# Performance work log

Measured on AMD Instinct MI355X. Metric: run time of the kernel, lower is better.

Reference implementation:

```python
import jax, jax.numpy as jnp
import numpy as np

N = 50000
E = 800000
D_IN, D_H1, D_H2, D_OUT = 128, 128, 64, 32


def setup_inputs() -> dict:
    key = jax.random.key(0)
    ks = jax.random.split(key, 8)
    x = jax.random.normal(ks[0], (N, D_IN), dtype=jnp.float32)
    edge_index = jax.random.randint(ks[1], (2, E), 0, N, dtype=jnp.int64)
    # Glorot-ish init for GCNConv weights, zero bias (PyG default bias init is zeros)
    def glorot(k, fi, fo):
        lim = np.sqrt(6.0 / (fi + fo)).astype(np.float32)
        return jax.random.uniform(k, (fi, fo), dtype=jnp.float32, minval=-lim, maxval=lim)
    return {
        "x": x,
        "edge_index": edge_index,
        "W1": glorot(ks[2], D_IN, D_H1), "b1": jnp.zeros((D_H1,), jnp.float32),
        "W2": glorot(ks[3], D_H1, D_H2), "b2": jnp.zeros((D_H2,), jnp.float32),
        "W3": glorot(ks[4], D_H2, D_OUT), "b3": jnp.zeros((D_OUT,), jnp.float32),
    }


def _gcn_norm(edge_index, n):
    # add self-loops, then symmetric normalization D^{-1/2} (A+I) D^{-1/2}
    loop = jnp.arange(n, dtype=edge_index.dtype)
    src = jnp.concatenate([edge_index[0], loop])  # [E+N]
    dst = jnp.concatenate([edge_index[1], loop])
    deg = jax.ops.segment_sum(jnp.ones_like(dst, dtype=jnp.float32), dst, num_segments=n)
    dinv = jnp.where(deg > 0, jax.lax.rsqrt(jnp.maximum(deg, 1.0)), 0.0)
    norm = dinv[src] * dinv[dst]  # [E+N]
    return src, dst, norm


def _gcn_layer(x, W, b, src, dst, norm, n):
    h = x @ W                                   # [N, d_out]
    msg = h[src] * norm[:, None]                # gather + scale, [E+N, d_out]
    agg = jax.ops.segment_sum(msg, dst, num_segments=n)
    return agg + b


def reference(x, edge_index, W1, b1, W2, b2, W3, b3):
    n = x.shape[0]
    src, dst, norm = _gcn_norm(edge_index, n)   # cached=True: computed once
    h = jax.nn.relu(_gcn_layer(x, W1, b1, src, dst, norm, n))
    h = jax.nn.relu(_gcn_layer(h, W2, b2, src, dst, norm, n))
    return _gcn_layer(h, W3, b3, src, dst, norm, n)
```

## Files before the change

### kernel.cpp

```cpp
#include <hip/hip_runtime.h>
#include <hip/hip_bf16.h>
#include <cstdint>

using short8 = __attribute__((ext_vector_type(8))) short;
using f32x4  = __attribute__((ext_vector_type(4))) float;

constexpr int CAP = 8192;

__device__ __forceinline__ unsigned f2bf_bits(float f) {
    unsigned u = __float_as_uint(f);
    return (u + 0x7fffu + ((u >> 16) & 1u)) >> 16;
}
__device__ __forceinline__ float bf_lo(unsigned u) { return __uint_as_float(u << 16); }
__device__ __forceinline__ float bf_hi(unsigned u) { return __uint_as_float(u & 0xffff0000u); }


__device__ __forceinline__ void prepack_one(const float* __restrict__ W,
                                            short* __restrict__ Wh, short* __restrict__ Wl,
                                            int DOUT, int idx) {
    int lane = idx & 63, tile = idx >> 6;
    int NT = DOUT / 16;
    int kk = tile / NT, ct = tile - kk * NT;
    int g = lane >> 4, cl = lane & 15;
    int c = ct * 16 + cl;
    short8 h8, l8;
#pragma unroll
    for (int j = 0; j < 8; ++j) {
        float w = W[(size_t)(kk * 32 + g * 8 + j) * DOUT + c];
        unsigned hb = f2bf_bits(w);
        unsigned lb = f2bf_bits(w - bf_lo(hb));
        h8[j] = (short)hb; l8[j] = (short)lb;
    }
    *reinterpret_cast<short8*>(&Wh[(size_t)idx * 8]) = h8;
    *reinterpret_cast<short8*>(&Wl[(size_t)idx * 8]) = l8;
}

__global__ __launch_bounds__(256) void prepack_all_kernel(const float* __restrict__ W1,
                                                          const float* __restrict__ W2,
                                                          const float* __restrict__ W3,
                                                          short* __restrict__ w1h, short* __restrict__ w1l,
                                                          short* __restrict__ w2h, short* __restrict__ w2l,
                                                          short* __restrict__ w3h, short* __restrict__ w3l,
                                                          int* __restrict__ bkt_cursor) {
    int idx = blockIdx.x * 256 + threadIdx.x;
    if (idx < 2048)      prepack_one(W1, w1h, w1l, 128, idx);
    else if (idx < 3072) prepack_one(W2, w2h, w2l, 64,  idx - 2048);
    else if (idx < 3328) prepack_one(W3, w3h, w3l, 32,  idx - 3072);
    else if (idx < 3584) bkt_cursor[idx - 3328] = 0;
}


struct BinSh {
    int qcnt[256];
    int qofs[256];
    int gbase[256];
    uint2 staging[4096];
};
struct GemmSh {
    unsigned Xh[64 * 64];
    unsigned Xl[64 * 64];
};
union SharedU { BinSh b; GemmSh g; };

__global__ __launch_bounds__(512) void bin_gemm1_kernel(const int* __restrict__ src,
                                                        const int* __restrict__ dst, int E,
                                                        int* __restrict__ bkt_cursor,
                                                        unsigned* __restrict__ bin,
                                                        const float* __restrict__ X,
                                                        const short8* __restrict__ Wp_hi,
                                                        const short8* __restrict__ Wp_lo,
                                                        unsigned* __restrict__ G,
                                                        int n, int NBE) {
    __shared__ SharedU sh;
    const int t = threadIdx.x;

    if ((int)blockIdx.x < NBE) {
        const int e0 = (int)blockIdx.x * 4096;
        if (t < 256) sh.b.qcnt[t] = 0;
        __syncthreads();
        int sa[8], da[8], slot[8];
#pragma unroll
        for (int k = 0; k < 8; ++k) {
            int e = e0 + k * 512 + t;
            sa[k] = -1; da[k] = 0; slot[k] = 0;
            if (e < E) {
                int ss = src[e], dd = dst[e];
                if (ss >= 0 && ss < n && dd >= 0 && dd < n) {
                    sa[k] = ss; da[k] = dd;
                    slot[k] = atomicAdd(&sh.b.qcnt[dd >> 8], 1);
                }
            }
        }
        __syncthreads();
        if (t < 256) sh.b.qofs[t] = sh.b.qcnt[t];
        __syncthreads();
        for (int off = 1; off < 256; off <<= 1) {
            int val = 0;
            if (t < 256 && t >= off) val = sh.b.qofs[t - off];
            __syncthreads();
            if (t < 256) sh.b.qofs[t] += val;
            __syncthreads();
        }
        if (t < 256) {
            int myc = sh.b.qcnt[t];
            if (myc > 0) sh.b.gbase[t] = atomicAdd(&bkt_cursor[t], myc);
            sh.b.qofs[t] -= myc;
        }
        __syncthreads();
#pragma unroll
        for (int k = 0; k < 8; ++k) {
            if (sa[k] >= 0)
                sh.b.staging[sh.b.qofs[da[k] >> 8] + slot[k]] =
                    make_uint2((unsigned)sa[k], (unsigned)da[k]);
        }
        __syncthreads();
        const int tot = sh.b.qofs[255] + sh.b.qcnt[255];
        for (int i = t; i < tot; i += 512) {
            uint2 en = sh.b.staging[i];
            int b = (int)(en.y >> 8);
            int pos = sh.b.gbase[b] + (i - sh.b.qofs[b]);
            if (pos < CAP)
                bin[(size_t)b * CAP + pos] = ((en.y & 255u) << 24) | en.x;
        }
        return;
    }

    constexpr int NT = 8, NTW = 4, NK = 4, WPR = 64;
    const int row0 = ((int)blockIdx.x - NBE) * 64;

    for (int i = t * 4; i < 64 * 128; i += 2048) {
        int r = i / 128, c = i % 128;
        float4 v = make_float4(0.f, 0.f, 0.f, 0.f);
        if (row0 + r < n) v = *reinterpret_cast<const float4*>(&X[(size_t)(row0 + r) * 128 + c]);
        unsigned h0 = f2bf_bits(v.x), h1 = f2bf_bits(v.y), h2 = f2bf_bits(v.z), h3 = f2bf_bits(v.w);
        unsigned l0 = f2bf_bits(v.x - bf_lo(h0)), l1 = f2bf_bits(v.y - bf_lo(h1));
        unsigned l2 = f2bf_bits(v.z - bf_lo(h2)), l3 = f2bf_bits(v.w - bf_lo(h3));
        int w = (r * WPR + c / 2) ^ ((r & 7) << 2);
        *reinterpret_cast<uint2*>(&sh.g.Xh[w]) = make_uint2(h0 | (h1 << 16), h2 | (h3 << 16));
        *reinterpret_cast<uint2*>(&sh.g.Xl[w]) = make_uint2(l0 | (l1 << 16), l2 | (l3 << 16));
    }
    __syncthreads();

    const int lane = t & 63, wid = t >> 6;
    const int strip = wid >> 1, half = wid & 1;
    const int g = lane >> 4, cl = lane & 15;
    const int lrow = strip * 16 + cl;
    f32x4 acc[NTW];
#pragma unroll
    for (int i = 0; i < NTW; ++i) acc[i] = (f32x4){0.f, 0.f, 0.f, 0.f};

#pragma unroll
    for (int kk = 0; kk < NK; ++kk) {
        int wb = (lrow * WPR + kk * 16 + g * 4) ^ ((lrow & 7) << 2);
        short8 xh = *reinterpret_cast<const short8*>(&sh.g.Xh[wb]);
        short8 xl = *reinterpret_cast<const short8*>(&sh.g.Xl[wb]);
#pragma unroll
        for (int i = 0; i < NTW; ++i) {
            int ct = half * NTW + i;
            short8 wh = Wp_hi[(kk * NT + ct) * 64 + lane];
            short8 wl = Wp_lo[(kk * NT + ct) * 64 + lane];
            acc[i] = __builtin_amdgcn_mfma_f32_16x16x32_bf16(wh, xh, acc[i], 0, 0, 0);
            acc[i] = __builtin_amdgcn_mfma_f32_16x16x32_bf16(wh, xl, acc[i], 0, 0, 0);
            acc[i] = __builtin_amdgcn_mfma_f32_16x16x32_bf16(wl, xh, acc[i], 0, 0, 0);
        }
    }

    const int r = row0 + lrow;
    if (r < n) {
#pragma unroll
        for (int i = 0; i < NTW; ++i) {
            int c0 = (half * NTW + i) * 16 + g * 4;
            unsigned p0 = f2bf_bits(acc[i][0]) | (f2bf_bits(acc[i][1]) << 16);
            unsigned p1 = f2bf_bits(acc[i][2]) | (f2bf_bits(acc[i][3]) << 16);
            *reinterpret_cast<uint2*>(&G[(size_t)r * 64 + c0 / 2]) = make_uint2(p0, p1);
        }
    }
}

__global__ __launch_bounds__(256) void bucket_offsets_fill_kernel(const unsigned* __restrict__ bin,
                                                                  const int* __restrict__ bkt_cursor,
                                                                  int2* __restrict__ off2,
                                                                  float* __restrict__ dinv,
                                                                  int* __restrict__ csr, int n) {
    __shared__ int cnt[256];
    __shared__ int sh[256];
    __shared__ int cur[256];
    const int t = threadIdx.x;
    const int b = blockIdx.x;
    const int S = b * CAP;
    const int count = min(bkt_cursor[b], CAP);
    cnt[t] = 0;
    __syncthreads();
    for (int i = t; i < count; i += 256) atomicAdd(&cnt[bin[S + i] >> 24], 1);
    __syncthreads();
    const int c = cnt[t];
    sh[t] = c;
    __syncthreads();
    for (int off = 1; off < 256; off <<= 1) {
        int val = (t >= off) ? sh[t - off] : 0;
        __syncthreads();
        sh[t] += val;
        __syncthreads();
    }
    const int start = S + sh[t] - c;
    cur[t] = start;
    const int node = b * 256 + t;
    if (node < n) {
        off2[node] = make_int2(start, start + c);
        dinv[node] = rsqrtf((float)(c + 1));
    }
    __syncthreads();
    for (int i = t; i < count; i += 256) {
        unsigned p = bin[S + i];
        int pos = atomicAdd(&cur[p >> 24], 1);
        csr[pos] = (int)(p & 0xFFFFFFu);
    }
}


template<int DIN, int DOUT, bool SCALE_IN>
__global__ __launch_bounds__(512) void fused_agg_gemm_kernel(const unsigned* __restrict__ Gin,
                                                             const int2* __restrict__ off2,
                                                             const int* __restrict__ csr,
                                                             const float* __restrict__ dinv,
                                                             const float* __restrict__ bias,
                                                             const short8* __restrict__ Wp_hi,
                                                             const short8* __restrict__ Wp_lo,
                                                             unsigned* __restrict__ Gout, int n) {
    constexpr int NT    = DOUT / 16;
    constexpr int NTW   = NT / 2;
    constexpr int NK    = DIN / 32;
    constexpr int WPR   = DIN / 2;
    constexpr int W4    = DIN / 8;
    constexpr int LPN   = W4;
    constexpr int SLOTS = 512 / LPN;
    constexpr int ROUNDS = 64 / SLOTS;
    __shared__ unsigned Xh[64 * WPR];
    __shared__ unsigned Xl[64 * WPR];
    const int t = threadIdx.x;
    const int node0 = blockIdx.x * 64;
    const int slot = t / LPN, cw = t % LPN;
    const uint4* gB = reinterpret_cast<const uint4*>(Gin) + cw;
    const int col = cw * 8;
    const float4 bs0 = *reinterpret_cast<const float4*>(&bias[col]);
    const float4 bs1 = *reinterpret_cast<const float4*>(&bias[col + 4]);

#pragma unroll
    for (int rd = 0; rd < ROUNDS; ++rd) {
        const int r = rd * SLOTS + slot;
        const int v = node0 + r;
        unsigned hw[4] = {0u, 0u, 0u, 0u}, lw[4] = {0u, 0u, 0u, 0u};
        if (v < n) {
            const float dv = dinv[v];
            float a[8], b[8];
            uint4 us = gB[(size_t)v * W4];
            const float sself = SCALE_IN ? dv : 1.f;
            a[0] = sself * bf_lo(us.x); a[1] = sself * bf_hi(us.x);
            a[2] = sself * bf_lo(us.y); a[3] = sself * bf_hi(us.y);
            a[4] = sself * bf_lo(us.z); a[5] = sself * bf_hi(us.z);
            a[6] = sself * bf_lo(us.w); a[7] = sself * bf_hi(us.w);
#pragma unroll
            for (int q = 0; q < 8; ++q) b[q] = 0.f;
            const int2 se = off2[v];
            int j = se.x;
            for (; j + 4 <= se.y; j += 4) {
                int u0 = csr[j], u1 = csr[j + 1], u2 = csr[j + 2], u3 = csr[j + 3];
                uint4 x0 = gB[(size_t)u0 * W4];
                uint4 x1 = gB[(size_t)u1 * W4];
                uint4 x2 = gB[(size_t)u2 * W4];
                uint4 x3 = gB[(size_t)u3 * W4];
                if (SCALE_IN) {
                    float w0 = dinv[u0], w1 = dinv[u1], w2 = dinv[u2], w3 = dinv[u3];
                    a[0] = fmaf(w0, bf_lo(x0.x), a[0]); a[1] = fmaf(w0, bf_hi(x0.x), a[1]);
                    a[2] = fmaf(w0, bf_lo(x0.y), a[2]); a[3] = fmaf(w0, bf_hi(x0.y), a[3]);
                    a[4] = fmaf(w0, bf_lo(x0.z), a[4]); a[5] = fmaf(w0, bf_hi(x0.z), a[5]);
                    a[6] = fmaf(w0, bf_lo(x0.w), a[6]); a[7] = fmaf(w0, bf_hi(x0.w), a[7]);
                    b[0] = fmaf(w1, bf_lo(x1.x), b[0]); b[1] = fmaf(w1, bf_hi(x1.x), b[1]);
                    b[2] = fmaf(w1, bf_lo(x1.y), b[2]); b[3] = fmaf(w1, bf_hi(x1.y), b[3]);
                    b[4] = fmaf(w1, bf_lo(x1.z), b[4]); b[5] = fmaf(w1, bf_hi(x1.z), b[5]);
                    b[6] = fmaf(w1, bf_lo(x1.w), b[6]); b[7] = fmaf(w1, bf_hi(x1.w), b[7]);
                    a[0] = fmaf(w2, bf_lo(x2.x), a[0]); a[1] = fmaf(w2, bf_hi(x2.x), a[1]);
                    a[2] = fmaf(w2, bf_lo(x2.y), a[2]); a[3] = fmaf(w2, bf_hi(x2.y), a[3]);
                    a[4] = fmaf(w2, bf_lo(x2.z), a[4]); a[5] = fmaf(w2, bf_hi(x2.z), a[5]);
                    a[6] = fmaf(w2, bf_lo(x2.w), a[6]); a[7] = fmaf(w2, bf_hi(x2.w), a[7]);
                    b[0] = fmaf(w3, bf_lo(x3.x), b[0]); b[1] = fmaf(w3, bf_hi(x3.x), b[1]);
                    b[2] = fmaf(w3, bf_lo(x3.y), b[2]); b[3] = fmaf(w3, bf_hi(x3.y), b[3]);
                    b[4] = fmaf(w3, bf_lo(x3.z), b[4]); b[5] = fmaf(w3, bf_hi(x3.z), b[5]);
                    b[6] = fmaf(w3, bf_lo(x3.w), b[6]); b[7] = fmaf(w3, bf_hi(x3.w), b[7]);
                } else {
                    a[0] += bf_lo(x0.x); a[1] += bf_hi(x0.x); a[2] += bf_lo(x0.y); a[3] += bf_hi(x0.y);
                    a[4] += bf_lo(x0.z); a[5] += bf_hi(x0.z); a[6] += bf_lo(x0.w); a[7] += bf_hi(x0.w);
                    b[0] += bf_lo(x1.x); b[1] += bf_hi(x1.x); b[2] += bf_lo(x1.y); b[3] += bf_hi(x1.y);
                    b[4] += bf_lo(x1.z); b[5] += bf_hi(x1.z); b[6] += bf_lo(x1.w); b[7] += bf_hi(x1.w);
                    a[0] += bf_lo(x2.x); a[1] += bf_hi(x2.x); a[2] += bf_lo(x2.y); a[3] += bf_hi(x2.y);
                    a[4] += bf_lo(x2.z); a[5] += bf_hi(x2.z); a[6] += bf_lo(x2.w); a[7] += bf_hi(x2.w);
                    b[0] += bf_lo(x3.x); b[1] += bf_hi(x3.x); b[2] += bf_lo(x3.y); b[3] += bf_hi(x3.y);
                    b[4] += bf_lo(x3.z); b[5] += bf_hi(x3.z); b[6] += bf_lo(x3.w); b[7] += bf_hi(x3.w);
                }
            }
            for (; j < se.y; ++j) {
                int u0 = csr[j];
                uint4 x0 = gB[(size_t)u0 * W4];
                if (SCALE_IN) {
                    float w0 = dinv[u0];
                    a[0] = fmaf(w0, bf_lo(x0.x), a[0]); a[1] = fmaf(w0, bf_hi(x0.x), a[1]);
                    a[2] = fmaf(w0, bf_lo(x0.y), a[2]); a[3] = fmaf(w0, bf_hi(x0.y), a[3]);
                    a[4] = fmaf(w0, bf_lo(x0.z), a[4]); a[5] = fmaf(w0, bf_hi(x0.z), a[5]);
                    a[6] = fmaf(w0, bf_lo(x0.w), a[6]); a[7] = fmaf(w0, bf_hi(x0.w), a[7]);
                } else {
                    a[0] += bf_lo(x0.x); a[1] += bf_hi(x0.x); a[2] += bf_lo(x0.y); a[3] += bf_hi(x0.y);
                    a[4] += bf_lo(x0.z); a[5] += bf_hi(x0.z); a[6] += bf_lo(x0.w); a[7] += bf_hi(x0.w);
                }
            }
            const float bb[8] = {bs0.x, bs0.y, bs0.z, bs0.w, bs1.x, bs1.y, bs1.z, bs1.w};
#pragma unroll
            for (int q = 0; q < 8; ++q) {
                float o = fmaxf(dv * (a[q] + b[q]) + bb[q], 0.f);
                unsigned hb = f2bf_bits(o);
                unsigned lb = f2bf_bits(o - bf_lo(hb));
                hw[q >> 1] |= (q & 1) ? (hb << 16) : hb;
                lw[q >> 1] |= (q & 1) ? (lb << 16) : lb;
            }
        }
        const int w0 = (r * WPR + cw * 4) ^ ((r & 7) << 2);
        *reinterpret_cast<uint4*>(&Xh[w0]) = make_uint4(hw[0], hw[1], hw[2], hw[3]);
        *reinterpret_cast<uint4*>(&Xl[w0]) = make_uint4(lw[0], lw[1], lw[2], lw[3]);
    }
    __syncthreads();

    const int lane = t & 63, wid = t >> 6;
    const int strip = wid >> 1, half = wid & 1;
    const int g = lane >> 4, cl = lane & 15;
    const int lrow = strip * 16 + cl;
    f32x4 acc[NTW];
#pragma unroll
    for (int i = 0; i < NTW; ++i) acc[i] = (f32x4){0.f, 0.f, 0.f, 0.f};

#pragma unroll
    for (int kk = 0; kk < NK; ++kk) {
        int wb = (lrow * WPR + kk * 16 + g * 4) ^ ((lrow & 7) << 2);
        short8 xh = *reinterpret_cast<const short8*>(&Xh[wb]);
        short8 xl = *reinterpret_cast<const short8*>(&Xl[wb]);
#pragma unroll
        for (int i = 0; i < NTW; ++i) {
            int ct = half * NTW + i;
            short8 wh = Wp_hi[(kk * NT + ct) * 64 + lane];
            short8 wl = Wp_lo[(kk * NT + ct) * 64 + lane];
            acc[i] = __builtin_amdgcn_mfma_f32_16x16x32_bf16(wh, xh, acc[i], 0, 0, 0);
            acc[i] = __builtin_amdgcn_mfma_f32_16x16x32_bf16(wh, xl, acc[i], 0, 0, 0);
            acc[i] = __builtin_amdgcn_mfma_f32_16x16x32_bf16(wl, xh, acc[i], 0, 0, 0);
        }
    }

    const int r = node0 + lrow;
    if (r < n) {
        const float s = dinv[r];
#pragma unroll
        for (int i = 0; i < NTW; ++i) {
            int c0 = (half * NTW + i) * 16 + g * 4;
            unsigned p0 = f2bf_bits(acc[i][0] * s) | (f2bf_bits(acc[i][1] * s) << 16);
            unsigned p1 = f2bf_bits(acc[i][2] * s) | (f2bf_bits(acc[i][3] * s) << 16);
            *reinterpret_cast<uint2*>(&Gout[(size_t)r * (DOUT / 2) + c0 / 2]) = make_uint2(p0, p1);
        }
    }
}


__global__ __launch_bounds__(256) void aggregate_final_kernel(const unsigned* __restrict__ G,
                                                              const int2* __restrict__ off2,
                                                              const int* __restrict__ csr,
                                                              const float* __restrict__ dinv,
                                                              const float* __restrict__ bias,
                                                              float* __restrict__ out, int n) {
    constexpr int D = 32, W2u = 8, LPN = 8;
    const int t = threadIdx.x;
    const int v = blockIdx.x * 32 + t / LPN;
    if (v >= n) return;
    const int cw = t % LPN;
    const uint2* gB = reinterpret_cast<const uint2*>(G) + cw;

    float a[4], b[4];
    uint2 us = gB[(size_t)v * W2u];
    a[0] = bf_lo(us.x); a[1] = bf_hi(us.x); a[2] = bf_lo(us.y); a[3] = bf_hi(us.y);
#pragma unroll
    for (int q = 0; q < 4; ++q) b[q] = 0.f;

    const int2 se = off2[v];
    int j = se.x;
    for (; j + 4 <= se.y; j += 4) {
        uint2 x0 = gB[(size_t)csr[j]     * W2u];
        uint2 x1 = gB[(size_t)csr[j + 1] * W2u];
        uint2 x2 = gB[(size_t)csr[j + 2] * W2u];
        uint2 x3 = gB[(size_t)csr[j + 3] * W2u];
        a[0] += bf_lo(x0.x); a[1] += bf_hi(x0.x); a[2] += bf_lo(x0.y); a[3] += bf_hi(x0.y);
        b[0] += bf_lo(x1.x); b[1] += bf_hi(x1.x); b[2] += bf_lo(x1.y); b[3] += bf_hi(x1.y);
        a[0] += bf_lo(x2.x); a[1] += bf_hi(x2.x); a[2] += bf_lo(x2.y); a[3] += bf_hi(x2.y);
        b[0] += bf_lo(x3.x); b[1] += bf_hi(x3.x); b[2] += bf_lo(x3.y); b[3] += bf_hi(x3.y);
    }
    for (; j < se.y; ++j) {
        uint2 x0 = gB[(size_t)csr[j] * W2u];
        a[0] += bf_lo(x0.x); a[1] += bf_hi(x0.x); a[2] += bf_lo(x0.y); a[3] += bf_hi(x0.y);
    }

    const float dv = dinv[v];
    const int col = cw * 4;
    const float4 bs = *reinterpret_cast<const float4*>(&bias[col]);
    float4 o = make_float4(dv * (a[0] + b[0]) + bs.x, dv * (a[1] + b[1]) + bs.y,
                           dv * (a[2] + b[2]) + bs.z, dv * (a[3] + b[3]) + bs.w);
    *reinterpret_cast<float4*>(&out[(size_t)v * D + col]) = o;
}


extern "C" void kernel_launch(void* const* d_in, const int* in_sizes, int n_in,
                              void* d_out, int out_size, void* d_ws, size_t ws_size,
                              hipStream_t stream) {
    const int N = 50000, E = 800000;
    const int NB  = (N + 255) / 256;
    const int NBE = (E + 4095) / 4096;
    const int NG  = (N + 63) / 64;
    const float* x  = (const float*)d_in[0];
    const int* ei = (const int*)d_in[1];
    const int* src = ei;
    const int* dst = ei + E;
    const float* W1 = (const float*)d_in[2]; const float* b1 = (const float*)d_in[3];
    const float* W2 = (const float*)d_in[4]; const float* b2 = (const float*)d_in[5];
    const float* W3 = (const float*)d_in[6]; const float* b3 = (const float*)d_in[7];
    float* out = (float*)d_out;

    char* ws = (char*)d_ws;
    size_t off = 0;
    auto alloc = [&](size_t bytes) -> void* {
        void* p = ws + off;
        off = (off + bytes + 255) & ~(size_t)255;
        return p;
    };
    int2*     off2       = (int2*)alloc((size_t)N * 8);
    float*    dinv       = (float*)alloc((size_t)N * 4);
    int*      csr        = (int*)alloc((size_t)NB * CAP * 4);
    unsigned* bin        = (unsigned*)alloc((size_t)NB * CAP * 4);
    unsigned* g1         = (unsigned*)alloc((size_t)N * 64 * 4);
    unsigned* g2         = (unsigned*)alloc((size_t)N * 32 * 4);
    unsigned* g3         = (unsigned*)alloc((size_t)N * 16 * 4);
    int*      bkt_cursor = (int*)alloc((size_t)256 * 4);
    short*    wp1h = (short*)alloc((size_t)128 * 128 * 2);
    short*    wp1l = (short*)alloc((size_t)128 * 128 * 2);
    short*    wp2h = (short*)alloc((size_t)128 * 64 * 2);
    short*    wp2l = (short*)alloc((size_t)128 * 64 * 2);
    short*    wp3h = (short*)alloc((size_t)64 * 32 * 2);
    short*    wp3l = (short*)alloc((size_t)64 * 32 * 2);
    (void)ws_size; (void)n_in; (void)in_sizes; (void)out_size;

    prepack_all_kernel<<<14, 256, 0, stream>>>(W1, W2, W3, wp1h, wp1l, wp2h, wp2l, wp3h, wp3l,
                                               bkt_cursor);
    bin_gemm1_kernel<<<NBE + NG, 512, 0, stream>>>(src, dst, E, bkt_cursor, bin,
                                                   x, (const short8*)wp1h, (const short8*)wp1l,
                                                   g1, N, NBE);
    bucket_offsets_fill_kernel<<<NB, 256, 0, stream>>>(bin, bkt_cursor, off2, dinv, csr, N);
    fused_agg_gemm_kernel<128, 64, true><<<NG, 512, 0, stream>>>(g1, off2, csr, dinv, b1,
                                                                 (const short8*)wp2h,
                                                                 (const short8*)wp2l, g2, N);
    fused_agg_gemm_kernel<64, 32, false><<<NG, 512, 0, stream>>>(g2, off2, csr, dinv, b2,
                                                                 (const short8*)wp3h,
                                                                 (const short8*)wp3l, g3, N);
    aggregate_final_kernel<<<(N * 8 + 255) / 256, 256, 0, stream>>>(g3, off2, csr, dinv, b3, out, N);
}
```

Measured before the change: 115.6 us.

## Prescale layer-1 features by dinv in bucket kernel; unroll gathers by eight

The bucket/offset kernel now multiplies each g1 row by its source-node dinv and writes it back as bf16, right after computing degrees. This removes the per-edge dinv gather and FMA scaling from the first fused aggregation, so both fused layers share one unscaled add path. The gather loops in the fused and final aggregation kernels are unrolled from 4 to 8 neighbours to keep more loads in flight. The cost is an extra read-modify-write pass over g1, a second bf16 rounding of the prescaled values, and higher register pressure from the wider unroll.

```diff
diff --git a/kernel.cpp b/kernel.cpp
--- a/kernel.cpp
+++ b/kernel.cpp
@@ -181,10 +181,12 @@
                                                                   const int* __restrict__ bkt_cursor,
                                                                   int2* __restrict__ off2,
                                                                   float* __restrict__ dinv,
-                                                                  int* __restrict__ csr, int n) {
+                                                                  int* __restrict__ csr,
+                                                                  unsigned* __restrict__ g1, int n) {
     __shared__ int cnt[256];
     __shared__ int sh[256];
     __shared__ int cur[256];
+    __shared__ float sdinv[256];
     const int t = threadIdx.x;
     const int b = blockIdx.x;
     const int S = b * CAP;
@@ -204,10 +206,13 @@
     }
     const int start = S + sh[t] - c;
     cur[t] = start;
-    const int node = b * 256 + t;
+    const float dv = rsqrtf((float)(c + 1));
+    sdinv[t] = dv;
+    const int node0 = b * 256;
+    const int node = node0 + t;
     if (node < n) {
         off2[node] = make_int2(start, start + c);
-        dinv[node] = rsqrtf((float)(c + 1));
+        dinv[node] = dv;
     }
     __syncthreads();
     for (int i = t; i < count; i += 256) {
@@ -215,10 +220,21 @@
         int pos = atomicAdd(&cur[p >> 24], 1);
         csr[pos] = (int)(p & 0xFFFFFFu);
     }
-}
-
-
-template<int DIN, int DOUT, bool SCALE_IN>
+    const int rows = min(256, n - node0);
+    uint4* g4 = reinterpret_cast<uint4*>(g1 + (size_t)node0 * 64);
+    for (int i = t; i < rows * 16; i += 256) {
+        const float s = sdinv[i >> 4];
+        uint4 v = g4[i];
+        unsigned r0 = f2bf_bits(s * bf_lo(v.x)) | (f2bf_bits(s * bf_hi(v.x)) << 16);
+        unsigned r1 = f2bf_bits(s * bf_lo(v.y)) | (f2bf_bits(s * bf_hi(v.y)) << 16);
+        unsigned r2 = f2bf_bits(s * bf_lo(v.z)) | (f2bf_bits(s * bf_hi(v.z)) << 16);
+        unsigned r3 = f2bf_bits(s * bf_lo(v.w)) | (f2bf_bits(s * bf_hi(v.w)) << 16);
+        g4[i] = make_uint4(r0, r1, r2, r3);
+    }
+}
+
+
+template<int DIN, int DOUT>
 __global__ __launch_bounds__(512) void fused_agg_gemm_kernel(const unsigned* __restrict__ Gin,
                                                              const int2* __restrict__ off2,
                                                              const int* __restrict__ csr,
@@ -251,67 +267,54 @@
         const int v = node0 + r;
         unsigned hw[4] = {0u, 0u, 0u, 0u}, lw[4] = {0u, 0u, 0u, 0u};
         if (v < n) {
-            const float dv = dinv[v];
             float a[8], b[8];
             uint4 us = gB[(size_t)v * W4];
-            const float sself = SCALE_IN ? dv : 1.f;
-            a[0] = sself * bf_lo(us.x); a[1] = sself * bf_hi(us.x);
-            a[2] = sself * bf_lo(us.y); a[3] = sself * bf_hi(us.y);
-            a[4] = sself * bf_lo(us.z); a[5] = sself * bf_hi(us.z);
-            a[6] = sself * bf_lo(us.w); a[7] = sself * bf_hi(us.w);
+            a[0] = bf_lo(us.x); a[1] = bf_hi(us.x); a[2] = bf_lo(us.y); a[3] = bf_hi(us.y);
+            a[4] = bf_lo(us.z); a[5] = bf_hi(us.z); a[6] = bf_lo(us.w); a[7] = bf_hi(us.w);
 #pragma unroll
             for (int q = 0; q < 8; ++q) b[q] = 0.f;
             const int2 se = off2[v];
             int j = se.x;
-            for (; j + 4 <= se.y; j += 4) {
-                int u0 = csr[j], u1 = csr[j + 1], u2 = csr[j + 2], u3 = csr[j + 3];
-                uint4 x0 = gB[(size_t)u0 * W4];
-                uint4 x1 = gB[(size_t)u1 * W4];
-                uint4 x2 = gB[(size_t)u2 * W4];
-                uint4 x3 = gB[(size_t)u3 * W4];
-                if (SCALE_IN) {
-                    float w0 = dinv[u0], w1 = dinv[u1], w2 = dinv[u2], w3 = dinv[u3];
-                    a[0] = fmaf(w0, bf_lo(x0.x), a[0]); a[1] = fmaf(w0, bf_hi(x0.x), a[1]);
-                    a[2] = fmaf(w0, bf_lo(x0.y), a[2]); a[3] = fmaf(w0, bf_hi(x0.y), a[3]);
-                    a[4] = fmaf(w0, bf_lo(x0.z), a[4]); a[5] = fmaf(w0, bf_hi(x0.z), a[5]);
-                    a[6] = fmaf(w0, bf_lo(x0.w), a[6]); a[7] = fmaf(w0, bf_hi(x0.w), a[7]);
-                    b[0] = fmaf(w1, bf_lo(x1.x), b[0]); b[1] = fmaf(w1, bf_hi(x1.x), b[1]);
-                    b[2] = fmaf(w1, bf_lo(x1.y), b[2]); b[3] = fmaf(w1, bf_hi(x1.y), b[3]);
-                    b[4] = fmaf(w1, bf_lo(x1.z), b[4]); b[5] = fmaf(w1, bf_hi(x1.z), b[5]);
-                    b[6] = fmaf(w1, bf_lo(x1.w), b[6]); b[7] = fmaf(w1, bf_hi(x1.w), b[7]);
-                    a[0] = fmaf(w2, bf_lo(x2.x), a[0]); a[1] = fmaf(w2, bf_hi(x2.x), a[1]);
-                    a[2] = fmaf(w2, bf_lo(x2.y), a[2]); a[3] = fmaf(w2, bf_hi(x2.y), a[3]);
-                    a[4] = fmaf(w2, bf_lo(x2.z), a[4]); a[5] = fmaf(w2, bf_hi(x2.z), a[5]);
-                    a[6] = fmaf(w2, bf_lo(x2.w), a[6]); a[7] = fmaf(w2, bf_hi(x2.w), a[7]);
-                    b[0] = fmaf(w3, bf_lo(x3.x), b[0]); b[1] = fmaf(w3, bf_hi(x3.x), b[1]);
-                    b[2] = fmaf(w3, bf_lo(x3.y), b[2]); b[3] = fmaf(w3, bf_hi(x3.y), b[3]);
-                    b[4] = fmaf(w3, bf_lo(x3.z), b[4]); b[5] = fmaf(w3, bf_hi(x3.z), b[5]);
-                    b[6] = fmaf(w3, bf_lo(x3.w), b[6]); b[7] = fmaf(w3, bf_hi(x3.w), b[7]);
-                } else {
-                    a[0] += bf_lo(x0.x); a[1] += bf_hi(x0.x); a[2] += bf_lo(x0.y); a[3] += bf_hi(x0.y);
-                    a[4] += bf_lo(x0.z); a[5] += bf_hi(x0.z); a[6] += bf_lo(x0.w); a[7] += bf_hi(x0.w);
-                    b[0] += bf_lo(x1.x); b[1] += bf_hi(x1.x); b[2] += bf_lo(x1.y); b[3] += bf_hi(x1.y);
-                    b[4] += bf_lo(x1.z); b[5] += bf_hi(x1.z); b[6] += bf_lo(x1.w); b[7] += bf_hi(x1.w);
-                    a[0] += bf_lo(x2.x); a[1] += bf_hi(x2.x); a[2] += bf_lo(x2.y); a[3] += bf_hi(x2.y);
-                    a[4] += bf_lo(x2.z); a[5] += bf_hi(x2.z); a[6] += bf_lo(x2.w); a[7] += bf_hi(x2.w);
-                    b[0] += bf_lo(x3.x); b[1] += bf_hi(x3.x); b[2] += bf_lo(x3.y); b[3] += bf_hi(x3.y);
-                    b[4] += bf_lo(x3.z); b[5] += bf_hi(x3.z); b[6] += bf_lo(x3.w); b[7] += bf_hi(x3.w);
-                }
+            for (; j + 8 <= se.y; j += 8) {
+                uint4 x0 = gB[(size_t)csr[j]     * W4];
+                uint4 x1 = gB[(size_t)csr[j + 1] * W4];
+                uint4 x2 = gB[(size_t)csr[j + 2] * W4];
+                uint4 x3 = gB[(size_t)csr[j + 3] * W4];
+                uint4 x4 = gB[(size_t)csr[j + 4] * W4];
+                uint4 x5 = gB[(size_t)csr[j + 5] * W4];
+                uint4 x6 = gB[(size_t)csr[j + 6] * W4];
+                uint4 x7 = gB[(size_t)csr[j + 7] * W4];
+                a[0] += bf_lo(x0.x); a[1] += bf_hi(x0.x); a[2] += bf_lo(x0.y); a[3] += bf_hi(x0.y);
+                a[4] += bf_lo(x0.z); a[5] += bf_hi(x0.z); a[6] += bf_lo(x0.w); a[7] += bf_hi(x0.w);
+                b[0] += bf_lo(x1.x); b[1] += bf_hi(x1.x); b[2] += bf_lo(x1.y); b[3] += bf_hi(x1.y);
+                b[4] += bf_lo(x1.z); b[5] += bf_hi(x1.z); b[6] += bf_lo(x1.w); b[7] += bf_hi(x1.w);
+                a[0] += bf_lo(x2.x); a[1] += bf_hi(x2.x); a[2] += bf_lo(x2.y); a[3] += bf_hi(x2.y);
+                a[4] += bf_lo(x2.z); a[5] += bf_hi(x2.z); a[6] += bf_lo(x2.w); a[7] += bf_hi(x2.w);
+                b[0] += bf_lo(x3.x); b[1] += bf_hi(x3.x); b[2] += bf_lo(x3.y); b[3] += bf_hi(x3.y);
+                b[4] += bf_lo(x3.z); b[5] += bf_hi(x3.z); b[6] += bf_lo(x3.w); b[7] += bf_hi(x3.w);
+                a[0] += bf_lo(x4.x); a[1] += bf_hi(x4.x); a[2] += bf_lo(x4.y); a[3] += bf_hi(x4.y);
+                a[4] += bf_lo(x4.z); a[5] += bf_hi(x4.z); a[6] += bf_lo(x4.w); a[7] += bf_hi(x4.w);
+                b[0] += bf_lo(x5.x); b[1] += bf_hi(x5.x); b[2] += bf_lo(x5.y); b[3] += bf_hi(x5.y);
+                b[4] += bf_lo(x5.z); b[5] += bf_hi(x5.z); b[6] += bf_lo(x5.w); b[7] += bf_hi(x5.w);
+                a[0] += bf_lo(x6.x); a[1] += bf_hi(x6.x); a[2] += bf_lo(x6.y); a[3] += bf_hi(x6.y);
+                a[4] += bf_lo(x6.z); a[5] += bf_hi(x6.z); a[6] += bf_lo(x6.w); a[7] += bf_hi(x6.w);
+                b[0] += bf_lo(x7.x); b[1] += bf_hi(x7.x); b[2] += bf_lo(x7.y); b[3] += bf_hi(x7.y);
+                b[4] += bf_lo(x7.z); b[5] += bf_hi(x7.z); b[6] += bf_lo(x7.w); b[7] += bf_hi(x7.w);
             }
-            for (; j < se.y; ++j) {
-                int u0 = csr[j];
-                uint4 x0 = gB[(size_t)u0 * W4];
-                if (SCALE_IN) {
-                    float w0 = dinv[u0];
-                    a[0] = fmaf(w0, bf_lo(x0.x), a[0]); a[1] = fmaf(w0, bf_hi(x0.x), a[1]);
-                    a[2] = fmaf(w0, bf_lo(x0.y), a[2]); a[3] = fmaf(w0, bf_hi(x0.y), a[3]);
-                    a[4] = fmaf(w0, bf_lo(x0.z), a[4]); a[5] = fmaf(w0, bf_hi(x0.z), a[5]);
-                    a[6] = fmaf(w0, bf_lo(x0.w), a[6]); a[7] = fmaf(w0, bf_hi(x0.w), a[7]);
-                } else {
-                    a[0] += bf_lo(x0.x); a[1] += bf_hi(x0.x); a[2] += bf_lo(x0.y); a[3] += bf_hi(x0.y);
-                    a[4] += bf_lo(x0.z); a[5] += bf_hi(x0.z); a[6] += bf_lo(x0.w); a[7] += bf_hi(x0.w);
-                }
+            for (; j + 2 <= se.y; j += 2) {
+                uint4 x0 = gB[(size_t)csr[j]     * W4];
+                uint4 x1 = gB[(size_t)csr[j + 1] * W4];
+                a[0] += bf_lo(x0.x); a[1] += bf_hi(x0.x); a[2] += bf_lo(x0.y); a[3] += bf_hi(x0.y);
+                a[4] += bf_lo(x0.z); a[5] += bf_hi(x0.z); a[6] += bf_lo(x0.w); a[7] += bf_hi(x0.w);
+                b[0] += bf_lo(x1.x); b[1] += bf_hi(x1.x); b[2] += bf_lo(x1.y); b[3] += bf_hi(x1.y);
+                b[4] += bf_lo(x1.z); b[5] += bf_hi(x1.z); b[6] += bf_lo(x1.w); b[7] += bf_hi(x1.w);
             }
+            if (j < se.y) {
+                uint4 x0 = gB[(size_t)csr[j] * W4];
+                a[0] += bf_lo(x0.x); a[1] += bf_hi(x0.x); a[2] += bf_lo(x0.y); a[3] += bf_hi(x0.y);
+                a[4] += bf_lo(x0.z); a[5] += bf_hi(x0.z); a[6] += bf_lo(x0.w); a[7] += bf_hi(x0.w);
+            }
+            const float dv = dinv[v];
             const float bb[8] = {bs0.x, bs0.y, bs0.z, bs0.w, bs1.x, bs1.y, bs1.z, bs1.w};
 #pragma unroll
             for (int q = 0; q < 8; ++q) {
@@ -387,15 +390,23 @@
 
     const int2 se = off2[v];
     int j = se.x;
-    for (; j + 4 <= se.y; j += 4) {
+    for (; j + 8 <= se.y; j += 8) {
         uint2 x0 = gB[(size_t)csr[j]     * W2u];
         uint2 x1 = gB[(size_t)csr[j + 1] * W2u];
         uint2 x2 = gB[(size_t)csr[j + 2] * W2u];
         uint2 x3 = gB[(size_t)csr[j + 3] * W2u];
+        uint2 x4 = gB[(size_t)csr[j + 4] * W2u];
+        uint2 x5 = gB[(size_t)csr[j + 5] * W2u];
+        uint2 x6 = gB[(size_t)csr[j + 6] * W2u];
+        uint2 x7 = gB[(size_t)csr[j + 7] * W2u];
         a[0] += bf_lo(x0.x); a[1] += bf_hi(x0.x); a[2] += bf_lo(x0.y); a[3] += bf_hi(x0.y);
         b[0] += bf_lo(x1.x); b[1] += bf_hi(x1.x); b[2] += bf_lo(x1.y); b[3] += bf_hi(x1.y);
         a[0] += bf_lo(x2.x); a[1] += bf_hi(x2.x); a[2] += bf_lo(x2.y); a[3] += bf_hi(x2.y);
         b[0] += bf_lo(x3.x); b[1] += bf_hi(x3.x); b[2] += bf_lo(x3.y); b[3] += bf_hi(x3.y);
+        a[0] += bf_lo(x4.x); a[1] += bf_hi(x4.x); a[2] += bf_lo(x4.y); a[3] += bf_hi(x4.y);
+        b[0] += bf_lo(x5.x); b[1] += bf_hi(x5.x); b[2] += bf_lo(x5.y); b[3] += bf_hi(x5.y);
+        a[0] += bf_lo(x6.x); a[1] += bf_hi(x6.x); a[2] += bf_lo(x6.y); a[3] += bf_hi(x6.y);
+        b[0] += bf_lo(x7.x); b[1] += bf_hi(x7.x); b[2] += bf_lo(x7.y); b[3] += bf_hi(x7.y);
     }
     for (; j < se.y; ++j) {
         uint2 x0 = gB[(size_t)csr[j] * W2u];
@@ -455,12 +466,12 @@
     bin_gemm1_kernel<<<NBE + NG, 512, 0, stream>>>(src, dst, E, bkt_cursor, bin,
                                                    x, (const short8*)wp1h, (const short8*)wp1l,
                                                    g1, N, NBE);
-    bucket_offsets_fill_kernel<<<NB, 256, 0, stream>>>(bin, bkt_cursor, off2, dinv, csr, N);
-    fused_agg_gemm_kernel<128, 64, true><<<NG, 512, 0, stream>>>(g1, off2, csr, dinv, b1,
-                                                                 (const short8*)wp2h,
-                                                                 (const short8*)wp2l, g2, N);
-    fused_agg_gemm_kernel<64, 32, false><<<NG, 512, 0, stream>>>(g2, off2, csr, dinv, b2,
-                                                                 (const short8*)wp3h,
-                                                                 (const short8*)wp3l, g3, N);
+    bucket_offsets_fill_kernel<<<NB, 256, 0, stream>>>(bin, bkt_cursor, off2, dinv, csr, g1, N);
+    fused_agg_gemm_kernel<128, 64><<<NG, 512, 0, stream>>>(g1, off2, csr, dinv, b1,
+                                                           (const short8*)wp2h,
+                                                           (const short8*)wp2l, g2, N);
+    fused_agg_gemm_kernel<64, 32><<<NG, 512, 0, stream>>>(g2, off2, csr, dinv, b2,
+                                                          (const short8*)wp3h,
+                                                          (const short8*)wp3l, g3, N);
     aggregate_final_kernel<<<(N * 8 + 255) / 256, 256, 0, stream>>>(g3, off2, csr, dinv, b3, out, N);
 }
```

Measured after the change: 117.5 us. Within noise of the previous version (+1.6%).
